# Optimization experiments

Measured on AMD Instinct MI355X. Metric: run time of the kernel, lower is better.

## Reference

```python
import jax, jax.numpy as jnp
import numpy as np

MIN_STD = 0.1

def _lin(x, W, b):
    return x @ W.T + b


def setup_inputs() -> dict:
    B, T, H, L, E, A = 256, 128, 2048, 256, 1024, 32
    key = jax.random.key(0)
    ks = jax.random.split(key, 40)
    def w(i, shape, s=0.02):
        return (jax.random.normal(ks[i], shape, jnp.float32) * s)
    z = lambda n: jnp.zeros((n,), jnp.float32)
    return {
        "prev_stochastic_state": w(0, (B, L), 1.0),
        "prev_hidden": w(1, (B, H), 1.0),
        "encoded_obs": w(2, (B, T, E), 1.0),
        "actions": w(3, (B, T, A), 1.0),
        "noise_prior": w(4, (B, T, L), 1.0),
        "noise_post": w(5, (B, T, L), 1.0),
        # fc_embed_state_action
        "W_embed": w(6, (H, L + A)), "b_embed": z(H),
        # GRUCell (torch layout: 3H rows = [r; z; n])
        "W_ih": w(7, (3 * H, H)), "b_ih": z(3 * H),
        "W_hh": w(8, (3 * H, H)), "b_hh": z(3 * H),
        # prior MLP (200-dim) + heads
        "Wp1": w(9, (200, H)), "bp1": z(200),
        "Wp2": w(10, (200, 200)), "bp2": z(200),
        "Wpm": w(11, (L, 200)), "bpm": z(L),
        "Wps": w(12, (L, 200)), "bps": z(L),
        # posterior MLP (200-dim) + heads
        "Wq1": w(13, (200, H + E)), "bq1": z(200),
        "Wq2": w(14, (200, 200)), "bq2": z(200),
        "Wqm": w(15, (L, 200)), "bqm": z(L),
        "Wqs": w(16, (L, 200)), "bqs": z(L),
        # reward head
        "Wr1": w(17, (200, L + H)), "br1": z(200),
        "Wr2": w(18, (200, 200)), "br2": z(200),
        "Wr3": w(19, (1, 200)), "br3": z(1),
    }


def reference(prev_stochastic_state, prev_hidden, encoded_obs, actions,
              noise_prior, noise_post,
              W_embed, b_embed, W_ih, b_ih, W_hh, b_hh,
              Wp1, bp1, Wp2, bp2, Wpm, bpm, Wps, bps,
              Wq1, bq1, Wq2, bq2, Wqm, bqm, Wqs, bqs,
              Wr1, br1, Wr2, br2, Wr3, br3):
    def gru(x, h):
        gi = x @ W_ih.T + b_ih          # [B, 3H]
        gh = h @ W_hh.T + b_hh
        i_r, i_z, i_n = jnp.split(gi, 3, axis=-1)
        h_r, h_z, h_n = jnp.split(gh, 3, axis=-1)
        r = jax.nn.sigmoid(i_r + h_r)
        z = jax.nn.sigmoid(i_z + h_z)
        n = jnp.tanh(i_n + r * h_n)
        return (1.0 - z) * n + z * h

    def step(carry, xs):
        post, h = carry
        enc_t, act_t, np_t, nq_t = xs
        emb = jax.nn.relu(_lin(jnp.concatenate([post, act_t], -1), W_embed, b_embed))
        h = gru(emb, h)
        pf = jax.nn.relu(_lin(jax.nn.relu(_lin(h, Wp1, bp1)), Wp2, bp2))
        pmu = _lin(pf, Wpm, bpm)
        pstd = jax.nn.softplus(_lin(pf, Wps, bps)) + MIN_STD
        prior_s = pmu + pstd * np_t
        qf = jax.nn.relu(_lin(jax.nn.relu(_lin(jnp.concatenate([h, enc_t], -1), Wq1, bq1)), Wq2, bq2))
        qmu = _lin(qf, Wqm, bqm)
        qstd = jax.nn.softplus(_lin(qf, Wqs, bqs)) + MIN_STD
        post = qmu + qstd * nq_t
        rew = _lin(jax.nn.relu(_lin(jax.nn.relu(_lin(jnp.concatenate([post, h], -1), Wr1, br1)), Wr2, br2)), Wr3, br3)
        return (post, h), (prior_s, post, h, pmu, pstd, qmu, qstd, rew)

    xs = (encoded_obs.transpose(1, 0, 2), actions.transpose(1, 0, 2),
          noise_prior.transpose(1, 0, 2), noise_post.transpose(1, 0, 2))
    _, ys = jax.lax.scan(step, (prev_stochastic_state, prev_hidden), xs)
    # scan stacks on axis 0 (time); torch stacks on dim 1 -> swap to [B, T, ...]
    return tuple(jnp.swapaxes(y, 0, 1) for y in ys)
```

## Files before the change

### kernel.cpp

```cpp
#include <hip/hip_runtime.h>
#include <hip/hip_bf16.h>

#define TS 128
#define NB 256
#define HD 2048
#define H3 6144
#define LD 256
#define ED 1024
#define AD 32
#define FD 200
#define KE 288
#define KQ 3072
#define KR 2304
#define MT 32768

typedef __attribute__((ext_vector_type(8))) short short8;
typedef __attribute__((ext_vector_type(4))) float f32x4;

constexpr size_t alup(size_t x) { return (x + 255) & ~size_t(255); }
constexpr size_t O_WE   = 0;
constexpr size_t O_WIH  = alup(O_WE   + 2ull*2048*288);
constexpr size_t O_WHH  = alup(O_WIH  + 2ull*6144*2048);
constexpr size_t O_WQ1  = alup(O_WHH  + 2ull*6144*2048);
constexpr size_t O_WQ2  = alup(O_WQ1  + 2ull*200*3072);
constexpr size_t O_WQMS = alup(O_WQ2  + 2ull*200*200);
constexpr size_t O_WP1  = alup(O_WQMS + 2ull*512*200);
constexpr size_t O_WP2  = alup(O_WP1  + 2ull*200*2048);
constexpr size_t O_WPMS = alup(O_WP2  + 2ull*200*200);
constexpr size_t O_WR1  = alup(O_WPMS + 2ull*512*200);
constexpr size_t O_WR2  = alup(O_WR1  + 2ull*200*2304);
constexpr size_t O_WR3  = alup(O_WR2  + 2ull*200*200);
constexpr size_t O_BQMS = alup(O_WR3  + 2ull*200);
constexpr size_t O_BPMS = alup(O_BQMS + 4ull*512);
constexpr size_t O_POSTB= alup(O_BPMS + 4ull*512);
constexpr size_t O_HB   = alup(O_POSTB+ 2ull*NB*LD);
constexpr size_t O_HF   = alup(O_HB   + 2ull*2*NB*HD);
constexpr size_t O_EMB  = alup(O_HF   + 4ull*2*NB*HD);
constexpr size_t O_Q1P  = alup(O_EMB  + 2ull*NB*HD);
constexpr size_t O_Q2   = alup(O_Q1P  + 4ull*4*NB*256);
constexpr size_t O_P1B  = alup(O_Q2   + 2ull*NB*FD);
constexpr size_t O_P2B  = alup(O_P1B  + 2ull*(size_t)MT*FD);
constexpr size_t O_END  = alup(O_P2B  + 2ull*(size_t)MT*FD);

#define Y0 0ull
#define Y1 8388608ull
#define Y2 16777216ull
#define Y3 83886080ull
#define Y4 92274688ull
#define Y5 100663296ull
#define Y6 109051904ull
#define Y7 117440512ull

__device__ __forceinline__ unsigned short f2bf(float f) {
  union { float f; unsigned u; } v; v.f = f;
  unsigned r = v.u + 0x7fffu + ((v.u >> 16) & 1u);
  return (unsigned short)(r >> 16);
}
__device__ __forceinline__ float bf2f(unsigned short u) {
  union { unsigned u; float f; } v; v.u = ((unsigned)u) << 16;
  return v.f;
}
__device__ __forceinline__ float sigm(float x) { return 1.f / (1.f + __expf(-x)); }
__device__ __forceinline__ float tanh_f(float x) {
  float e = __expf(-2.f * fabsf(x));
  float t = (1.f - e) / (1.f + e);
  return x >= 0.f ? t : -t;
}
__device__ __forceinline__ float softp(float x) { return x > 15.f ? x : log1pf(__expf(x)); }
__device__ __forceinline__ f32x4 z4() { f32x4 z; z[0]=0.f; z[1]=0.f; z[2]=0.f; z[3]=0.f; return z; }

struct SMem {
  alignas(16) short As[64*72];
  alignas(16) short Ws[128*72];
};
struct SMemG {
  alignas(16) short A[3][64*64];
  alignas(16) short W[3][64*64];
};

struct Aseg {
  const char* p0; int lda0; int K0; int f0;
  const char* p1; int lda1; int f1;
  int K;
};

__device__ __forceinline__ void stageA(short* As, const Aseg& a, int m0, int k0) {
  const int t = threadIdx.x;
  const int row = t >> 2;
  const int cb = (t & 3) << 4;
  #pragma unroll
  for (int i = 0; i < 2; ++i) {
    const int c = cb + i * 8;
    const int gk = k0 + c;
    short8 v = {};
    if (gk < a.K) {
      const char* p; long idx; int isf;
      if (gk < a.K0) { p = a.p0; idx = (long)(m0 + row) * a.lda0 + gk; isf = a.f0; }
      else           { p = a.p1; idx = (long)(m0 + row) * a.lda1 + (gk - a.K0); isf = a.f1; }
      if (isf) {
        const float* pf = (const float*)p + idx;
        #pragma unroll
        for (int j = 0; j < 8; ++j) v[j] = (short)f2bf(pf[j]);
      } else {
        v = *(const short8*)((const short*)p + idx);
      }
    }
    *(short8*)&As[row*72 + c] = v;
  }
}

__device__ __forceinline__ void stageW(short* Ws, const short* W, int ldw, int n0, int BN,
                                       int Nmax, int k0, int K) {
  const int nch = BN << 3;
  for (int id = threadIdx.x; id < nch; id += 256) {
    const int row = id >> 3;
    const int c = (id & 7) << 3;
    const int gk = k0 + c;
    int gr = n0 + row; gr = gr < Nmax ? gr : Nmax - 1;
    short8 v = {};
    if (gk < K) v = *(const short8*)(W + (long)gr * ldw + gk);
    *(short8*)&Ws[row*72 + c] = v;
  }
}

__device__ __forceinline__ void stageA_red(short* As, const float* q1p, const float* bq1,
                                           int m0, int k0) {
  const int t = threadIdx.x;
  const int row = t >> 2;
  const int cb = (t & 3) << 4;
  #pragma unroll
  for (int i = 0; i < 2; ++i) {
    const int c = cb + i * 8;
    const int gk = k0 + c;
    short8 v = {};
    if (gk < FD) {
      float s[8];
      #pragma unroll
      for (int j = 0; j < 8; ++j) s[j] = bq1[gk + j];
      #pragma unroll
      for (int ss = 0; ss < 4; ++ss) {
        const float* p = q1p + (size_t)ss * NB * 256 + (size_t)(m0 + row) * 256 + gk;
        #pragma unroll
        for (int j = 0; j < 8; ++j) s[j] += p[j];
      }
      #pragma unroll
      for (int j = 0; j < 8; ++j) v[j] = (short)f2bf(fmaxf(s[j], 0.f));
    }
    *(short8*)&As[row*72 + c] = v;
  }
}

template<int NF>
__device__ __forceinline__ void mma_tile(const short* As, const short* Ws, f32x4 acc[2][NF]) {
  const int lane = threadIdx.x & 63;
  const int w = threadIdx.x >> 6;
  const int wm = (w >> 1) << 5;
  const int wn = (w & 1) * (NF << 4);
  const int lr = lane & 15, lk = (lane >> 4) << 3;
  #pragma unroll
  for (int ks = 0; ks < 2; ++ks) {
    const int ko = ks * 32 + lk;
    short8 a0 = *(const short8*)&As[(wm + lr)*72 + ko];
    short8 a1 = *(const short8*)&As[(wm + 16 + lr)*72 + ko];
    #pragma unroll
    for (int f = 0; f < NF; ++f) {
      short8 b = *(const short8*)&Ws[(wn + f*16 + lr)*72 + ko];
      acc[0][f] = __builtin_amdgcn_mfma_f32_16x16x32_bf16(a0, b, acc[0][f], 0, 0, 0);
      acc[1][f] = __builtin_amdgcn_mfma_f32_16x16x32_bf16(a1, b, acc[1][f], 0, 0, 0);
    }
  }
}

template<int NF>
__device__ void run_gemm(SMem& sm, const Aseg& a, const short* W, int ldw, int m0, int n0,
                         int Nmax, f32x4 acc[2][NF], int kb, int ke) {
  for (int k0 = kb; k0 < ke; k0 += 64) {
    __syncthreads();
    stageA(sm.As, a, m0, k0);
    stageW(sm.Ws, W, ldw, n0, NF*32, Nmax, k0, a.K);
    __syncthreads();
    mma_tile<NF>(sm.As, sm.Ws, acc);
  }
}

template<int NF>
__device__ void epi_generic(f32x4 acc[2][NF], int m0, int n0, int Nmax, const float* bias,
                            int relu, float* outF, long rsF, unsigned short* outB, int rsB) {
  const int lane = threadIdx.x & 63;
  const int w = threadIdx.x >> 6;
  const int wm = (w >> 1) << 5, wn = (w & 1) * (NF << 4);
  #pragma unroll
  for (int mt = 0; mt < 2; ++mt)
  #pragma unroll
  for (int f = 0; f < NF; ++f)
  #pragma unroll
  for (int r = 0; r < 4; ++r) {
    const int m = m0 + wm + mt*16 + ((lane >> 4) << 2) + r;
    const int n = n0 + wn + f*16 + (lane & 15);
    if (n < Nmax) {
      float v = acc[mt][f][r];
      if (bias) v += bias[n];
      if (relu) v = fmaxf(v, 0.f);
      if (outF) outF[(long)m * rsF + n] = v;
      if (outB) outB[(long)m * rsB + n] = f2bf(v);
    }
  }
}

template<int NF>
__device__ void epi_heads(f32x4 acc[2][NF], int m0, int n0, const float* biasI,
                          const float* noise, long rs, float* outMu, float* outStd,
                          float* outComb, unsigned short* postbf) {
  const int lane = threadIdx.x & 63;
  const int w = threadIdx.x >> 6;
  const int wm = (w >> 1) << 5, wn = (w & 1) * (NF << 4);
  #pragma unroll
  for (int mt = 0; mt < 2; ++mt)
  #pragma unroll
  for (int f = 0; f < NF; ++f)
  #pragma unroll
  for (int r = 0; r < 4; ++r) {
    const int m = m0 + wm + mt*16 + ((lane >> 4) << 2) + r;
    const int n = n0 + wn + f*16 + (lane & 15);
    float v = acc[mt][f][r] + biasI[n];
    if (n & 1) v = softp(v) + 0.1f;
    float partner = __shfl_xor(v, 1);
    const int l = n >> 1;
    if (n & 1) {
      outStd[(long)m * rs + l] = v;
    } else {
      outMu[(long)m * rs + l] = v;
      float comb = v + partner * noise[(long)m * rs + l];
      outComb[(long)m * rs + l] = comb;
      if (postbf) postbf[m * LD + l] = f2bf(comb);
    }
  }
}

__device__ __forceinline__ void gl_lds16(const void* g, void* l) {
  __builtin_amdgcn_global_load_lds(
      (const __attribute__((address_space(1))) unsigned int*)g,
      (__attribute__((address_space(3))) unsigned int*)l, 16, 0, 0);
}

__device__ __forceinline__ void stage64(short* dst, const short* g, long ldw,
                                        int rbase, int k0) {
  const int w = threadIdx.x >> 6, l = threadIdx.x & 63;
  #pragma unroll
  for (int i = 0; i < 2; ++i) {
    const int inst = w*2 + i;
    const int row = inst*8 + (l >> 3);
    const int sc = (l & 7) ^ (row & 7);
    gl_lds16(g + (long)(rbase + row) * ldw + k0 + sc*8, dst + inst*512);
  }
}
__device__ __forceinline__ void stage_gi(short* dst, const short* W, int j0, int k0) {
  const int w = threadIdx.x >> 6, l = threadIdx.x & 63;
  #pragma unroll
  for (int i = 0; i < 2; ++i) {
    const int inst = w*2 + i;
    const int row = inst*8 + (l >> 3);
    const int g = (row >> 4) % 3;
    const int sc = (l & 7) ^ (row & 7);
    gl_lds16(W + (long)(g*2048 + j0 + (row & 15)) * 2048 + k0 + sc*8, dst + inst*512);
  }
}

__device__ __forceinline__ void mma_gi(const short* As, const short* Ws, f32x4 acc[3]) {
  const int lane = threadIdx.x & 63, w = threadIdx.x >> 6;
  const int lr = lane & 15, lk = (lane >> 4) << 3;
  #pragma unroll
  for (int ks = 0; ks < 2; ++ks) {
    const int ko = ks*32 + lk; const int ca = ko >> 3;
    const int ra = w*16 + lr;
    short8 av = *(const short8*)&As[ra*64 + ((ca ^ (ra & 7)) << 3)];
    #pragma unroll
    for (int f = 0; f < 3; ++f) {
      const int rb = f*16 + lr;
      short8 bv = *(const short8*)&Ws[rb*64 + ((ca ^ (rb & 7)) << 3)];
      acc[f] = __builtin_amdgcn_mfma_f32_16x16x32_bf16(av, bv, acc[f], 0, 0, 0);
    }
  }
}

struct CArgs {
  char* ws;
  const float* enc; const float* act; const float* nq;
  const float* b_e; const float* b_ih; const float* b_hh;
  const float* b_q1; const float* b_q2;
  float* y1; float* y2; float* y5; float* y6;
};

__device__ __forceinline__ void gruf_stage(SMemG& sm, int buf, int idx,
    const short* hB, const short* eB, const short* Whh, const short* Wih,
    int m0, int j0) {
  const short* Ab; const short* Wb; int k0;
  if (idx < 32) { Ab = hB; Wb = Whh; k0 = idx*64; }
  else          { Ab = eB; Wb = Wih; k0 = (idx-32)*64; }
  stage64(sm.A[buf], Ab, HD, m0, k0);
  stage_gi(sm.W[buf], Wb, j0, k0);
}

__global__ __launch_bounds__(256, 2) void k_gruf(CArgs A, int t) {
  __shared__ SMemG sm;
  const int id = blockIdx.x;
  const int xcd = id & 7, local = id >> 3;
  const int mi = local & 3, jl = local >> 2;
  const int m0 = mi << 6, j0 = xcd*256 + jl*16;
  const int p = t & 1;
  const short* hB  = (const short*)(A.ws + O_HB) + (size_t)p*NB*HD;
  const short* eB  = (const short*)(A.ws + O_EMB);
  const short* Whh = (const short*)(A.ws + O_WHH);
  const short* Wih = (const short*)(A.ws + O_WIH);
  f32x4 ah[3], ai[3];
  #pragma unroll
  for (int f = 0; f < 3; ++f) { ah[f] = z4(); ai[f] = z4(); }

  gruf_stage(sm, 0, 0, hB, eB, Whh, Wih, m0, j0);
  gruf_stage(sm, 1, 1, hB, eB, Whh, Wih, m0, j0);
  #pragma unroll 1
  for (int idx = 0; idx < 64; ++idx) {
    const int buf = idx % 3;
    if (idx + 2 < 64) {
      gruf_stage(sm, (idx + 2) % 3, idx + 2, hB, eB, Whh, Wih, m0, j0);
      asm volatile("s_waitcnt vmcnt(8)" ::: "memory");
    } else if (idx + 1 < 64) {
      asm volatile("s_waitcnt vmcnt(4)" ::: "memory");
    } else {
      asm volatile("s_waitcnt vmcnt(0)" ::: "memory");
    }
    __builtin_amdgcn_s_barrier();
    __builtin_amdgcn_sched_barrier(0);
    if (idx < 32) mma_gi(sm.A[buf], sm.W[buf], ah);
    else          mma_gi(sm.A[buf], sm.W[buf], ai);
    asm volatile("s_waitcnt lgkmcnt(0)" ::: "memory");
    __builtin_amdgcn_sched_barrier(0);
    __builtin_amdgcn_s_barrier();
  }

  const int lane = threadIdx.x & 63, w = threadIdx.x >> 6;
  const int lr = lane & 15;
  const int j = j0 + lr;
  const float* hFo = (const float*)(A.ws + O_HF) + (size_t)p*NB*HD;
  float*       hFn = (float*)(A.ws + O_HF) + (size_t)(p^1)*NB*HD;
  unsigned short* hBn = (unsigned short*)(A.ws + O_HB) + (size_t)(p^1)*NB*HD;
  #pragma unroll
  for (int r = 0; r < 4; ++r) {
    const int m = m0 + w*16 + ((lane >> 4) << 2) + r;
    const float ir = ai[0][r] + A.b_ih[j]        + ah[0][r] + A.b_hh[j];
    const float iz = ai[1][r] + A.b_ih[HD + j]   + ah[1][r] + A.b_hh[HD + j];
    const float in_ = ai[2][r] + A.b_ih[2*HD + j];
    const float hn  = ah[2][r] + A.b_hh[2*HD + j];
    const float rr = sigm(ir), zz = sigm(iz);
    const float nn = tanh_f(in_ + rr * hn);
    const float hv = (1.f - zz) * nn + zz * hFo[(size_t)m*HD + j];
    hFn[(size_t)m*HD + j] = hv;
    hBn[(size_t)m*HD + j] = f2bf(hv);
    A.y2[(size_t)m * (TS*HD) + (size_t)t*HD + j] = hv;
  }
}

__global__ __launch_bounds__(256, 2) void k_emb(CArgs A, int t) {
  __shared__ SMem sm;
  const int id = blockIdx.x;
  const int mi = id & 3, ni = id >> 2;
  const int m0 = mi << 6, n0 = ni << 7;
  Aseg a{A.ws + O_POSTB, LD, LD, 0, (const char*)(A.act + (size_t)t*AD), TS*AD, 1, KE};
  f32x4 acc[2][4];
  for (int i=0;i<2;++i) for (int j=0;j<4;++j) acc[i][j] = z4();
  run_gemm<4>(sm, a, (const short*)(A.ws + O_WE), KE, m0, n0, HD, acc, 0, 320);
  epi_generic<4>(acc, m0, n0, HD, A.b_e, 1, nullptr, 0, (unsigned short*)(A.ws + O_EMB), HD);
}

__global__ __launch_bounds__(256, 2) void k_q1(CArgs A, int t) {
  __shared__ SMem sm;
  const int id = blockIdx.x;
  const int s = id >> 3, rest = id & 7;
  const int mi = rest & 3, ni = rest >> 2;
  const int m0 = mi << 6, n0 = ni << 7;
  const short* hB = (const short*)(A.ws + O_HB) + (size_t)((t+1)&1)*NB*HD;
  Aseg a{(const char*)hB, HD, HD, 0, (const char*)(A.enc + (size_t)t*ED), TS*ED, 1, KQ};
  f32x4 acc[2][4];
  for (int i=0;i<2;++i) for (int j=0;j<4;++j) acc[i][j] = z4();
  run_gemm<4>(sm, a, (const short*)(A.ws + O_WQ1), KQ, m0, n0, FD, acc, s*768, s*768+768);
  epi_generic<4>(acc, m0, n0, FD, nullptr, 0,
                 (float*)(A.ws + O_Q1P) + (size_t)s*NB*256, 256, nullptr, 0);
}

__global__ __launch_bounds__(256, 2) void k_q2(CArgs A) {
  __shared__ SMem sm;
  const int id = blockIdx.x;
  const int mi = id & 3, ni = id >> 2;
  const int m0 = mi << 6, n0 = ni << 7;
  f32x4 acc[2][4];
  for (int i=0;i<2;++i) for (int j=0;j<4;++j) acc[i][j] = z4();
  const short* W = (const short*)(A.ws + O_WQ2);
  for (int k0 = 0; k0 < 256; k0 += 64) {
    __syncthreads();
    stageA_red(sm.As, (const float*)(A.ws + O_Q1P), A.b_q1, m0, k0);
    stageW(sm.Ws, W, FD, n0, 128, FD, k0, FD);
    __syncthreads();
    mma_tile<4>(sm.As, sm.Ws, acc);
  }
  epi_generic<4>(acc, m0, n0, FD, A.b_q2, 1, nullptr, 0, (unsigned short*)(A.ws + O_Q2), FD);
}

__global__ __launch_bounds__(256, 2) void k_heads(CArgs A, int t) {
  __shared__ SMem sm;
  const int id = blockIdx.x;
  const int mi = id & 3, ni = id >> 2;
  const int m0 = mi << 6, n0 = ni << 7;
  Aseg a{A.ws + O_Q2, FD, FD, 0, nullptr, 0, 0, FD};
  f32x4 acc[2][4];
  for (int i=0;i<2;++i) for (int j=0;j<4;++j) acc[i][j] = z4();
  run_gemm<4>(sm, a, (const short*)(A.ws + O_WQMS), FD, m0, n0, 512, acc, 0, 256);
  epi_heads<4>(acc, m0, n0, (const float*)(A.ws + O_BQMS),
               A.nq + (size_t)t*LD, (long)TS*LD,
               A.y5 + (size_t)t*LD, A.y6 + (size_t)t*LD, A.y1 + (size_t)t*LD,
               (unsigned short*)(A.ws + O_POSTB));
}

__global__ void k_init(char* ws, const float* prevs, const float* prevh,
  const float* We, const float* Wih, const float* Whh,
  const float* Wp1, const float* Wp2, const float* Wpm, const float* Wps,
  const float* Wq1, const float* Wq2, const float* Wqm, const float* Wqs,
  const float* Wr1, const float* Wr2, const float* Wr3,
  const float* bpm, const float* bps, const float* bqm, const float* bqs) {
  const size_t stride = (size_t)gridDim.x * blockDim.x;
  for (size_t i = (size_t)blockIdx.x*blockDim.x + threadIdx.x; i < 12582912ull; i += stride) {
    ((unsigned short*)(ws + O_WIH))[i] = f2bf(Wih[i]);
    ((unsigned short*)(ws + O_WHH))[i] = f2bf(Whh[i]);
    if (i < 589824)  ((unsigned short*)(ws + O_WE))[i]  = f2bf(We[i]);
    if (i < 614400)  ((unsigned short*)(ws + O_WQ1))[i] = f2bf(Wq1[i]);
    if (i < 409600)  ((unsigned short*)(ws + O_WP1))[i] = f2bf(Wp1[i]);
    if (i < 460800)  ((unsigned short*)(ws + O_WR1))[i] = f2bf(Wr1[i]);
    if (i < 40000) {
      ((unsigned short*)(ws + O_WQ2))[i] = f2bf(Wq2[i]);
      ((unsigned short*)(ws + O_WP2))[i] = f2bf(Wp2[i]);
      ((unsigned short*)(ws + O_WR2))[i] = f2bf(Wr2[i]);
    }
    if (i < 200) ((unsigned short*)(ws + O_WR3))[i] = f2bf(Wr3[i]);
    if (i < 102400) {
      const int r = (int)(i / 200), c = (int)(i % 200);
      ((unsigned short*)(ws + O_WQMS))[i] = f2bf(((r & 1) ? Wqs : Wqm)[(r >> 1)*200 + c]);
      ((unsigned short*)(ws + O_WPMS))[i] = f2bf(((r & 1) ? Wps : Wpm)[(r >> 1)*200 + c]);
    }
    if (i < 512) {
      ((float*)(ws + O_BQMS))[i] = ((i & 1) ? bqs : bqm)[i >> 1];
      ((float*)(ws + O_BPMS))[i] = ((i & 1) ? bps : bpm)[i >> 1];
    }
    if (i < 65536) ((unsigned short*)(ws + O_POSTB))[i] = f2bf(prevs[i]);
    if (i < 524288) {
      ((unsigned short*)(ws + O_HB))[i] = f2bf(prevh[i]);
      ((float*)(ws + O_HF))[i] = prevh[i];
    }
  }
}

__global__ __launch_bounds__(256, 2) void k_big(int mode, char* ws,
  const float* y1, const float* y2, float* y0, float* y3, float* y4,
  const float* npn, const float* bp1, const float* bp2, const float* br1, const float* br2) {
  __shared__ SMem sm;
  if (mode == 2) {
    for (int tile = blockIdx.x; tile < 2048; tile += gridDim.x) {
      const int mi = tile >> 2, ni = tile & 3;
      const int m0 = mi << 6, n0 = ni << 7;
      Aseg a{ws + O_P2B, FD, FD, 0, nullptr, 0, 0, FD};
      f32x4 acc[2][4];
      for (int i=0;i<2;++i) for (int j=0;j<4;++j) acc[i][j] = z4();
      run_gemm<4>(sm, a, (const short*)(ws + O_WPMS), FD, m0, n0, 512, acc, 0, 256);
      epi_heads<4>(acc, m0, n0, (const float*)(ws + O_BPMS), npn, 256, y3, y4, y0, nullptr);
    }
    return;
  }
  for (int tile = blockIdx.x; tile < 1024; tile += gridDim.x) {
    const int mi = tile >> 1, ni = tile & 1;
    const int m0 = mi << 6, n0 = ni << 7;
    Aseg a; const short* W; const float* bias;
    if (mode == 0)      { a = {(const char*)y2, HD, HD, 1, nullptr, 0, 0, HD}; W = (const short*)(ws + O_WP1); bias = bp1; }
    else if (mode == 1) { a = {ws + O_P1B, FD, FD, 0, nullptr, 0, 0, FD};      W = (const short*)(ws + O_WP2); bias = bp2; }
    else if (mode == 3) { a = {(const char*)y1, LD, LD, 1, (const char*)y2, HD, 1, KR}; W = (const short*)(ws + O_WR1); bias = br1; }
    else                { a = {ws + O_P1B, FD, FD, 0, nullptr, 0, 0, FD};      W = (const short*)(ws + O_WR2); bias = br2; }
    f32x4 acc[2][4];
    for (int i=0;i<2;++i) for (int j=0;j<4;++j) acc[i][j] = z4();
    const int ke = (a.K + 63) & ~63;
    run_gemm<4>(sm, a, W, a.K, m0, n0, FD, acc, 0, ke);
    unsigned short* outp = (unsigned short*)(ws + ((mode == 0 || mode == 3) ? O_P1B : O_P2B));
    epi_generic<4>(acc, m0, n0, FD, bias, 1, nullptr, 0, outp, FD);
  }
}

__global__ void k_r3(char* ws, const float* br3, float* y7) {
  __shared__ float w3[200];
  for (int i = threadIdx.x; i < 200; i += 256) w3[i] = bf2f(((unsigned short*)(ws + O_WR3))[i]);
  __syncthreads();
  const int m = blockIdx.x * 256 + threadIdx.x;
  const unsigned short* r2 = (const unsigned short*)(ws + O_P2B) + (size_t)m * FD;
  float s = br3[0];
  for (int k = 0; k < FD; k += 8) {
    short8 v = *(const short8*)(r2 + k);
    #pragma unroll
    for (int j = 0; j < 8; ++j) s += bf2f((unsigned short)v[j]) * w3[k + j];
  }
  y7[m] = s;
}

extern "C" void kernel_launch(void* const* d_in, const int* in_sizes, int n_in,
                              void* d_out, int out_size, void* d_ws, size_t ws_size,
                              hipStream_t stream) {
  (void)in_sizes; (void)n_in; (void)out_size; (void)ws_size;
  char* ws = (char*)d_ws;
  #define FIN(i) ((const float*)d_in[i])
  float* out = (float*)d_out;
  float* y0 = out + Y0; float* y1 = out + Y1; float* y2 = out + Y2; float* y3 = out + Y3;
  float* y4 = out + Y4; float* y5 = out + Y5; float* y6 = out + Y6; float* y7 = out + Y7;

  k_init<<<2048, 256, 0, stream>>>(ws, FIN(0), FIN(1), FIN(6), FIN(8), FIN(10),
    FIN(12), FIN(14), FIN(16), FIN(18), FIN(20), FIN(22), FIN(24), FIN(26),
    FIN(28), FIN(30), FIN(32), FIN(17), FIN(19), FIN(25), FIN(27));

  CArgs ca;
  ca.ws = ws; ca.enc = FIN(2); ca.act = FIN(3); ca.nq = FIN(5);
  ca.b_e = FIN(7); ca.b_ih = FIN(9); ca.b_hh = FIN(11); ca.b_q1 = FIN(21); ca.b_q2 = FIN(23);
  ca.y1 = y1; ca.y2 = y2; ca.y5 = y5; ca.y6 = y6;

  for (int t = 0; t < TS; ++t) {
    k_emb  <<<64,  256, 0, stream>>>(ca, t);
    k_gruf <<<512, 256, 0, stream>>>(ca, t);
    k_q1   <<<32,  256, 0, stream>>>(ca, t);
    k_q2   <<<8,   256, 0, stream>>>(ca);
    k_heads<<<16,  256, 0, stream>>>(ca, t);
  }

  k_big<<<2048, 256, 0, stream>>>(0, ws, y1, y2, y0, y3, y4, FIN(4), FIN(13), FIN(15), FIN(29), FIN(31));
  k_big<<<2048, 256, 0, stream>>>(1, ws, y1, y2, y0, y3, y4, FIN(4), FIN(13), FIN(15), FIN(29), FIN(31));
  k_big<<<2048, 256, 0, stream>>>(2, ws, y1, y2, y0, y3, y4, FIN(4), FIN(13), FIN(15), FIN(29), FIN(31));
  k_big<<<2048, 256, 0, stream>>>(3, ws, y1, y2, y0, y3, y4, FIN(4), FIN(13), FIN(15), FIN(29), FIN(31));
  k_big<<<2048, 256, 0, stream>>>(4, ws, y1, y2, y0, y3, y4, FIN(4), FIN(13), FIN(15), FIN(29), FIN(31));
  k_r3<<<128, 256, 0, stream>>>(ws, FIN(33), y7);
}
```

Before: 17.27 ms.

## Split GRU hidden GEMM off critical path and fuse posterior chain per step

The recurrent h@W_hh GEMM is moved into a separate pass that runs alongside a new fused per-row-block chain kernel (q1, q2, heads, next-step embedding), and it stores gh to a workspace buffer. The input-gate kernel then reads gh and only computes x@W_ih, using a W_ih layout permuted at init so each block streams contiguous rows. This cuts per-step launches from five to two and overlaps independent work, aiming to shorten the sequential critical path. In exchange it adds a large fp32 gh buffer that must be written and re-read every step, and the chain kernel uses few small blocks with long serial K loops.

```diff
diff --git a/kernel.cpp b/kernel.cpp
--- a/kernel.cpp
+++ b/kernel.cpp
@@ -36,9 +36,8 @@
 constexpr size_t O_HB   = alup(O_POSTB+ 2ull*NB*LD);
 constexpr size_t O_HF   = alup(O_HB   + 2ull*2*NB*HD);
 constexpr size_t O_EMB  = alup(O_HF   + 4ull*2*NB*HD);
-constexpr size_t O_Q1P  = alup(O_EMB  + 2ull*NB*HD);
-constexpr size_t O_Q2   = alup(O_Q1P  + 4ull*4*NB*256);
-constexpr size_t O_P1B  = alup(O_Q2   + 2ull*NB*FD);
+constexpr size_t O_GH   = alup(O_EMB  + 2ull*NB*HD);
+constexpr size_t O_P1B  = alup(O_GH   + 4ull*NB*H3);
 constexpr size_t O_P2B  = alup(O_P1B  + 2ull*(size_t)MT*FD);
 constexpr size_t O_END  = alup(O_P2B  + 2ull*(size_t)MT*FD);
 
@@ -77,6 +76,18 @@
   alignas(16) short A[3][64*64];
   alignas(16) short W[3][64*64];
 };
+struct SMemGi {
+  alignas(16) short A[3][64*64];
+  alignas(16) short W[3][48*64];
+};
+struct ChainC {
+  alignas(16) short Ws[256*40];
+  alignas(16) short q1f[16*264];
+  alignas(16) short q2f[16*264];
+  alignas(16) short postb[16*264];
+};
+union ChainSM { SMemG g; ChainC c; };
+union ProSM   { SMemG g; SMem legacy; };
 
 struct Aseg {
   const char* p0; int lda0; int K0; int f0;
@@ -123,33 +134,6 @@
   }
 }
 
-__device__ __forceinline__ void stageA_red(short* As, const float* q1p, const float* bq1,
-                                           int m0, int k0) {
-  const int t = threadIdx.x;
-  const int row = t >> 2;
-  const int cb = (t & 3) << 4;
-  #pragma unroll
-  for (int i = 0; i < 2; ++i) {
-    const int c = cb + i * 8;
-    const int gk = k0 + c;
-    short8 v = {};
-    if (gk < FD) {
-      float s[8];
-      #pragma unroll
-      for (int j = 0; j < 8; ++j) s[j] = bq1[gk + j];
-      #pragma unroll
-      for (int ss = 0; ss < 4; ++ss) {
-        const float* p = q1p + (size_t)ss * NB * 256 + (size_t)(m0 + row) * 256 + gk;
-        #pragma unroll
-        for (int j = 0; j < 8; ++j) s[j] += p[j];
-      }
-      #pragma unroll
-      for (int j = 0; j < 8; ++j) v[j] = (short)f2bf(fmaxf(s[j], 0.f));
-    }
-    *(short8*)&As[row*72 + c] = v;
-  }
-}
-
 template<int NF>
 __device__ __forceinline__ void mma_tile(const short* As, const short* Ws, f32x4 acc[2][NF]) {
   const int lane = threadIdx.x & 63;
@@ -254,15 +238,35 @@
     gl_lds16(g + (long)(rbase + row) * ldw + k0 + sc*8, dst + inst*512);
   }
 }
-__device__ __forceinline__ void stage_gi(short* dst, const short* W, int j0, int k0) {
+__device__ __forceinline__ void stage_giW(short* dst, const short* WX, int k0) {
   const int w = threadIdx.x >> 6, l = threadIdx.x & 63;
   #pragma unroll
-  for (int i = 0; i < 2; ++i) {
-    const int inst = w*2 + i;
-    const int row = inst*8 + (l >> 3);
-    const int g = (row >> 4) % 3;
+  for (int ii = 0; ii < 2; ++ii) {
+    const int i = (w < 3 ? w*2 : 4) + ii;
+    const int row = i*8 + (l >> 3);
     const int sc = (l & 7) ^ (row & 7);
-    gl_lds16(W + (long)(g*2048 + j0 + (row & 15)) * 2048 + k0 + sc*8, dst + inst*512);
+    gl_lds16(WX + (long)row * 2048 + k0 + sc*8, dst + i*512);
+  }
+}
+
+template<int NF>
+__device__ __forceinline__ void mma_swz(const short* As, const short* Ws, f32x4 acc[2][NF]) {
+  const int lane = threadIdx.x & 63, w = threadIdx.x >> 6;
+  const int wm = (w >> 1) << 5, wn = (w & 1) * (NF << 4);
+  const int lr = lane & 15, lk = (lane >> 4) << 3;
+  #pragma unroll
+  for (int ks = 0; ks < 2; ++ks) {
+    const int ko = ks*32 + lk; const int ca = ko >> 3;
+    const int ra0 = wm + lr, ra1 = wm + 16 + lr;
+    short8 a0 = *(const short8*)&As[ra0*64 + ((ca ^ (ra0 & 7)) << 3)];
+    short8 a1 = *(const short8*)&As[ra1*64 + ((ca ^ (ra1 & 7)) << 3)];
+    #pragma unroll
+    for (int f = 0; f < NF; ++f) {
+      const int rb = wn + f*16 + lr;
+      short8 b = *(const short8*)&Ws[rb*64 + ((ca ^ (rb & 7)) << 3)];
+      acc[0][f] = __builtin_amdgcn_mfma_f32_16x16x32_bf16(a0, b, acc[0][f], 0, 0, 0);
+      acc[1][f] = __builtin_amdgcn_mfma_f32_16x16x32_bf16(a1, b, acc[1][f], 0, 0, 0);
+    }
   }
 }
 
@@ -291,48 +295,64 @@
   float* y1; float* y2; float* y5; float* y6;
 };
 
-__device__ __forceinline__ void gruf_stage(SMemG& sm, int buf, int idx,
-    const short* hB, const short* eB, const short* Whh, const short* Wih,
-    int m0, int j0) {
-  const short* Ab; const short* Wb; int k0;
-  if (idx < 32) { Ab = hB; Wb = Whh; k0 = idx*64; }
-  else          { Ab = eB; Wb = Wih; k0 = (idx-32)*64; }
-  stage64(sm.A[buf], Ab, HD, m0, k0);
-  stage_gi(sm.W[buf], Wb, j0, k0);
-}
-
-__global__ __launch_bounds__(256, 2) void k_gruf(CArgs A, int t) {
-  __shared__ SMemG sm;
+__device__ void gh_pipe(SMemG& sm, const short* hB, const short* Whh, int m0, int n0,
+                        const float* bhh, float* ghout) {
+  f32x4 acc[2][2];
+  for (int i=0;i<2;++i) for (int j=0;j<2;++j) acc[i][j] = z4();
+  stage64(sm.A[0], hB, HD, m0, 0);   stage64(sm.W[0], Whh, HD, n0, 0);
+  stage64(sm.A[1], hB, HD, m0, 64);  stage64(sm.W[1], Whh, HD, n0, 64);
+  #pragma unroll 1
+  for (int idx = 0; idx < 32; ++idx) {
+    const int buf = idx % 3;
+    if (idx + 2 < 32) {
+      const int nb = (idx + 2) % 3;
+      stage64(sm.A[nb], hB, HD, m0, (idx+2)*64);
+      stage64(sm.W[nb], Whh, HD, n0, (idx+2)*64);
+      asm volatile("s_waitcnt vmcnt(8)" ::: "memory");
+    } else if (idx + 1 < 32) {
+      asm volatile("s_waitcnt vmcnt(4)" ::: "memory");
+    } else {
+      asm volatile("s_waitcnt vmcnt(0)" ::: "memory");
+    }
+    __builtin_amdgcn_s_barrier();
+    __builtin_amdgcn_sched_barrier(0);
+    mma_swz<2>(sm.A[buf], sm.W[buf], acc);
+    asm volatile("s_waitcnt lgkmcnt(0)" ::: "memory");
+    __builtin_amdgcn_sched_barrier(0);
+    __builtin_amdgcn_s_barrier();
+  }
+  epi_generic<2>(acc, m0, n0, H3, bhh, 0, ghout, H3, nullptr, 0);
+}
+
+__global__ __launch_bounds__(256, 2) void k_gi(CArgs A, int t) {
+  __shared__ SMemGi sm;
   const int id = blockIdx.x;
   const int xcd = id & 7, local = id >> 3;
   const int mi = local & 3, jl = local >> 2;
   const int m0 = mi << 6, j0 = xcd*256 + jl*16;
   const int p = t & 1;
-  const short* hB  = (const short*)(A.ws + O_HB) + (size_t)p*NB*HD;
   const short* eB  = (const short*)(A.ws + O_EMB);
-  const short* Whh = (const short*)(A.ws + O_WHH);
-  const short* Wih = (const short*)(A.ws + O_WIH);
-  f32x4 ah[3], ai[3];
-  #pragma unroll
-  for (int f = 0; f < 3; ++f) { ah[f] = z4(); ai[f] = z4(); }
-
-  gruf_stage(sm, 0, 0, hB, eB, Whh, Wih, m0, j0);
-  gruf_stage(sm, 1, 1, hB, eB, Whh, Wih, m0, j0);
+  const short* WX  = (const short*)(A.ws + O_WIH) + (size_t)(xcd*16 + jl)*48*2048;
+  f32x4 ai[3]; ai[0] = z4(); ai[1] = z4(); ai[2] = z4();
+
+  stage64(sm.A[0], eB, HD, m0, 0);   stage_giW(sm.W[0], WX, 0);
+  stage64(sm.A[1], eB, HD, m0, 64);  stage_giW(sm.W[1], WX, 64);
   #pragma unroll 1
-  for (int idx = 0; idx < 64; ++idx) {
+  for (int idx = 0; idx < 32; ++idx) {
     const int buf = idx % 3;
-    if (idx + 2 < 64) {
-      gruf_stage(sm, (idx + 2) % 3, idx + 2, hB, eB, Whh, Wih, m0, j0);
+    if (idx + 2 < 32) {
+      const int nb = (idx + 2) % 3;
+      stage64(sm.A[nb], eB, HD, m0, (idx+2)*64);
+      stage_giW(sm.W[nb], WX, (idx+2)*64);
       asm volatile("s_waitcnt vmcnt(8)" ::: "memory");
-    } else if (idx + 1 < 64) {
+    } else if (idx + 1 < 32) {
       asm volatile("s_waitcnt vmcnt(4)" ::: "memory");
     } else {
       asm volatile("s_waitcnt vmcnt(0)" ::: "memory");
     }
     __builtin_amdgcn_s_barrier();
     __builtin_amdgcn_sched_barrier(0);
-    if (idx < 32) mma_gi(sm.A[buf], sm.W[buf], ah);
-    else          mma_gi(sm.A[buf], sm.W[buf], ai);
+    mma_gi(sm.A[buf], sm.W[buf], ai);
     asm volatile("s_waitcnt lgkmcnt(0)" ::: "memory");
     __builtin_amdgcn_sched_barrier(0);
     __builtin_amdgcn_s_barrier();
@@ -344,15 +364,16 @@
   const float* hFo = (const float*)(A.ws + O_HF) + (size_t)p*NB*HD;
   float*       hFn = (float*)(A.ws + O_HF) + (size_t)(p^1)*NB*HD;
   unsigned short* hBn = (unsigned short*)(A.ws + O_HB) + (size_t)(p^1)*NB*HD;
+  const float* gh = (const float*)(A.ws + O_GH);
   #pragma unroll
   for (int r = 0; r < 4; ++r) {
     const int m = m0 + w*16 + ((lane >> 4) << 2) + r;
-    const float ir = ai[0][r] + A.b_ih[j]        + ah[0][r] + A.b_hh[j];
-    const float iz = ai[1][r] + A.b_ih[HD + j]   + ah[1][r] + A.b_hh[HD + j];
+    const float* g = gh + (size_t)m * H3;
+    const float ir  = ai[0][r] + A.b_ih[j]        + g[j];
+    const float iz  = ai[1][r] + A.b_ih[HD + j]   + g[HD + j];
     const float in_ = ai[2][r] + A.b_ih[2*HD + j];
-    const float hn  = ah[2][r] + A.b_hh[2*HD + j];
     const float rr = sigm(ir), zz = sigm(iz);
-    const float nn = tanh_f(in_ + rr * hn);
+    const float nn = tanh_f(in_ + rr * g[2*HD + j]);
     const float hv = (1.f - zz) * nn + zz * hFo[(size_t)m*HD + j];
     hFn[(size_t)m*HD + j] = hv;
     hBn[(size_t)m*HD + j] = f2bf(hv);
@@ -360,64 +381,222 @@
   }
 }
 
-__global__ __launch_bounds__(256, 2) void k_emb(CArgs A, int t) {
-  __shared__ SMem sm;
+struct W4 { short8 v[4]; };
+
+__device__ __forceinline__ void ldW(W4& r, const short* W, int ldw, int n0, int Nmax,
+                                    int k0, int K) {
+  const int tid = threadIdx.x;
+  #pragma unroll
+  for (int q = 0; q < 4; ++q) {
+    const int ch = q*256 + tid;
+    const int row = ch >> 2;
+    int gr = n0 + row; gr = gr < Nmax ? gr : Nmax - 1;
+    const int gk = k0 + (ch & 3) * 8;
+    short8 v = {};
+    if (gk < K) v = *(const short8*)(W + (long)gr*ldw + gk);
+    r.v[q] = v;
+  }
+}
+__device__ __forceinline__ void stW(short* Ws, const W4& r) {
+  const int tid = threadIdx.x;
+  #pragma unroll
+  for (int q = 0; q < 4; ++q) {
+    const int ch = q*256 + tid;
+    *(short8*)&Ws[(ch >> 2)*40 + (ch & 3)*8] = r.v[q];
+  }
+}
+
+template<int PH>
+__device__ __forceinline__ short8 ldA_chain(const CArgs& A, const short* lds,
+                                            const short* hB2, int m0, int t, int k0) {
+  const int lane = threadIdx.x & 63;
+  const int lr = lane & 15;
+  const int kk = k0 + ((lane >> 4) << 3);
+  if (PH == 1) {
+    if (kk < 2048) return *(const short8*)(hB2 + (long)(m0 + lr)*HD + kk);
+    const float* ep = A.enc + ((size_t)(m0 + lr)*TS + t)*ED + (kk - 2048);
+    f32x4 a = *(const f32x4*)ep;
+    f32x4 b = *(const f32x4*)(ep + 4);
+    short8 rv;
+    #pragma unroll
+    for (int j = 0; j < 4; ++j) { rv[j] = (short)f2bf(a[j]); rv[4+j] = (short)f2bf(b[j]); }
+    return rv;
+  }
+  if (PH == 4) {
+    if (kk < 256) return *(const short8*)&lds[lr*264 + kk];
+    const float* ap = A.act + ((size_t)(m0 + lr)*TS + (t + 1))*AD + (kk - 256);
+    f32x4 a = *(const f32x4*)ap;
+    f32x4 b = *(const f32x4*)(ap + 4);
+    short8 rv;
+    #pragma unroll
+    for (int j = 0; j < 4; ++j) { rv[j] = (short)f2bf(a[j]); rv[4+j] = (short)f2bf(b[j]); }
+    return rv;
+  }
+  return *(const short8*)&lds[lr*264 + kk];
+}
+
+__device__ __forceinline__ void mma_chain(const short* Ws, short8 af, f32x4 acc[4]) {
+  const int lane = threadIdx.x & 63, w = threadIdx.x >> 6;
+  const int lr = lane & 15;
+  #pragma unroll
+  for (int f = 0; f < 4; ++f) {
+    const int rb = w*64 + f*16 + lr;
+    short8 b = *(const short8*)&Ws[rb*40 + ((lane >> 4) << 3)];
+    acc[f] = __builtin_amdgcn_mfma_f32_16x16x32_bf16(af, b, acc[f], 0, 0, 0);
+  }
+}
+
+template<int PH>
+__device__ void chain_gemm(const CArgs& A, short* Ws, const short* aLDS, const short* hB2,
+                           int m0, int t, const short* W, int ldw, int Nmax,
+                           int S, int K, int n0, f32x4 acc[4]) {
+  W4 wrA, wrB;
+  ldW(wrA, W, ldw, n0, Nmax, 0, K);
+  if (S > 1) ldW(wrB, W, ldw, n0, Nmax, 32, K);
+  short8 af = ldA_chain<PH>(A, aLDS, hB2, m0, t, 0);
+  for (int s = 0; s < S; s += 2) {
+    {
+      __syncthreads();
+      stW(Ws, wrA);
+      __syncthreads();
+      if (s + 2 < S) ldW(wrA, W, ldw, n0, Nmax, (s+2)*32, K);
+      short8 afn = af;
+      if (s + 1 < S) afn = ldA_chain<PH>(A, aLDS, hB2, m0, t, (s+1)*32);
+      mma_chain(Ws, af, acc);
+      __builtin_amdgcn_sched_barrier(0);
+      af = afn;
+    }
+    if (s + 1 < S) {
+      __syncthreads();
+      stW(Ws, wrB);
+      __syncthreads();
+      if (s + 3 < S) ldW(wrB, W, ldw, n0, Nmax, (s+3)*32, K);
+      short8 afn = af;
+      if (s + 2 < S) afn = ldA_chain<PH>(A, aLDS, hB2, m0, t, (s+2)*32);
+      mma_chain(Ws, af, acc);
+      __builtin_amdgcn_sched_barrier(0);
+      af = afn;
+    }
+  }
+}
+
+__device__ __forceinline__ void epi_lds200(f32x4 acc[4], const float* bias, short* dst) {
+  const int lane = threadIdx.x & 63, w = threadIdx.x >> 6;
+  #pragma unroll
+  for (int f = 0; f < 4; ++f)
+  #pragma unroll
+  for (int r = 0; r < 4; ++r) {
+    const int n = w*64 + f*16 + (lane & 15);
+    const int mrow = ((lane >> 4) << 2) + r;
+    float v = acc[f][r] + (n < FD ? bias[n] : 0.f);
+    v = fmaxf(v, 0.f);
+    dst[mrow*264 + n] = (n < FD) ? (short)f2bf(v) : (short)0;
+  }
+}
+
+__global__ __launch_bounds__(256, 2) void k_chain(CArgs A, int t) {
+  __shared__ ChainSM sm;
   const int id = blockIdx.x;
-  const int mi = id & 3, ni = id >> 2;
-  const int m0 = mi << 6, n0 = ni << 7;
-  Aseg a{A.ws + O_POSTB, LD, LD, 0, (const char*)(A.act + (size_t)t*AD), TS*AD, 1, KE};
-  f32x4 acc[2][4];
-  for (int i=0;i<2;++i) for (int j=0;j<4;++j) acc[i][j] = z4();
-  run_gemm<4>(sm, a, (const short*)(A.ws + O_WE), KE, m0, n0, HD, acc, 0, 320);
-  epi_generic<4>(acc, m0, n0, HD, A.b_e, 1, nullptr, 0, (unsigned short*)(A.ws + O_EMB), HD);
-}
-
-__global__ __launch_bounds__(256, 2) void k_q1(CArgs A, int t) {
-  __shared__ SMem sm;
+  const int p2 = (t + 1) & 1;
+  const short* hB2 = (const short*)(A.ws + O_HB) + (size_t)p2*NB*HD;
+
+  if (id < 384) {
+    if (t == TS - 1) return;
+    const int xcd = id & 7, local = id >> 3;
+    const int mi = local & 3, nio = local >> 2;
+    const int m0 = mi << 6, n0 = xcd*768 + nio*64;
+    gh_pipe(sm.g, hB2, (const short*)(A.ws + O_WHH), m0, n0, A.b_hh,
+            (float*)(A.ws + O_GH));
+    return;
+  }
+
+  const int m0 = (id - 384) << 4;
+  short* Ws    = sm.c.Ws;
+  short* q1f   = sm.c.q1f;
+  short* q2f   = sm.c.q2f;
+  short* postb = sm.c.postb;
+  const int lane = threadIdx.x & 63, w = threadIdx.x >> 6;
+  f32x4 acc[4];
+
+  for (int f = 0; f < 4; ++f) acc[f] = z4();
+  chain_gemm<1>(A, Ws, nullptr, hB2, m0, t, (const short*)(A.ws + O_WQ1), KQ, FD, 96, KQ, 0, acc);
+  epi_lds200(acc, A.b_q1, q1f);
+  __syncthreads();
+
+  for (int f = 0; f < 4; ++f) acc[f] = z4();
+  chain_gemm<2>(A, Ws, q1f, hB2, m0, t, (const short*)(A.ws + O_WQ2), FD, FD, 7, FD, 0, acc);
+  epi_lds200(acc, A.b_q2, q2f);
+  __syncthreads();
+
+  const float* bqms = (const float*)(A.ws + O_BQMS);
+  #pragma unroll 1
+  for (int nc = 0; nc < 2; ++nc) {
+    for (int f = 0; f < 4; ++f) acc[f] = z4();
+    chain_gemm<3>(A, Ws, q2f, hB2, m0, t, (const short*)(A.ws + O_WQMS), FD, 512, 7, FD, nc*256, acc);
+    #pragma unroll
+    for (int f = 0; f < 4; ++f)
+    #pragma unroll
+    for (int r = 0; r < 4; ++r) {
+      const int n = nc*256 + w*64 + f*16 + (lane & 15);
+      const int mrow = ((lane >> 4) << 2) + r;
+      const int m = m0 + mrow;
+      float v = acc[f][r] + bqms[n];
+      if (n & 1) v = softp(v) + 0.1f;
+      float partner = __shfl_xor(v, 1);
+      const int l = n >> 1;
+      const size_t base = (size_t)m*TS*LD + (size_t)t*LD + l;
+      if (n & 1) {
+        A.y6[base] = v;
+      } else {
+        A.y5[base] = v;
+        float comb = v + partner * A.nq[base];
+        A.y1[base] = comb;
+        postb[mrow*264 + l] = (short)f2bf(comb);
+      }
+    }
+    __syncthreads();
+  }
+
+  if (t + 1 < TS) {
+    unsigned short* embp = (unsigned short*)(A.ws + O_EMB);
+    #pragma unroll 1
+    for (int nc = 0; nc < 8; ++nc) {
+      for (int f = 0; f < 4; ++f) acc[f] = z4();
+      chain_gemm<4>(A, Ws, postb, hB2, m0, t, (const short*)(A.ws + O_WE), KE, HD, 9, KE, nc*256, acc);
+      #pragma unroll
+      for (int f = 0; f < 4; ++f)
+      #pragma unroll
+      for (int r = 0; r < 4; ++r) {
+        const int n = nc*256 + w*64 + f*16 + (lane & 15);
+        const int mrow = ((lane >> 4) << 2) + r;
+        float v = acc[f][r] + A.b_e[n];
+        v = fmaxf(v, 0.f);
+        embp[(size_t)(m0 + mrow)*HD + n] = f2bf(v);
+      }
+      __syncthreads();
+    }
+  }
+}
+
+__global__ __launch_bounds__(256, 2) void k_pro(CArgs A) {
+  __shared__ ProSM sm;
   const int id = blockIdx.x;
-  const int s = id >> 3, rest = id & 7;
-  const int mi = rest & 3, ni = rest >> 2;
-  const int m0 = mi << 6, n0 = ni << 7;
-  const short* hB = (const short*)(A.ws + O_HB) + (size_t)((t+1)&1)*NB*HD;
-  Aseg a{(const char*)hB, HD, HD, 0, (const char*)(A.enc + (size_t)t*ED), TS*ED, 1, KQ};
-  f32x4 acc[2][4];
-  for (int i=0;i<2;++i) for (int j=0;j<4;++j) acc[i][j] = z4();
-  run_gemm<4>(sm, a, (const short*)(A.ws + O_WQ1), KQ, m0, n0, FD, acc, s*768, s*768+768);
-  epi_generic<4>(acc, m0, n0, FD, nullptr, 0,
-                 (float*)(A.ws + O_Q1P) + (size_t)s*NB*256, 256, nullptr, 0);
-}
-
-__global__ __launch_bounds__(256, 2) void k_q2(CArgs A) {
-  __shared__ SMem sm;
-  const int id = blockIdx.x;
-  const int mi = id & 3, ni = id >> 2;
-  const int m0 = mi << 6, n0 = ni << 7;
-  f32x4 acc[2][4];
-  for (int i=0;i<2;++i) for (int j=0;j<4;++j) acc[i][j] = z4();
-  const short* W = (const short*)(A.ws + O_WQ2);
-  for (int k0 = 0; k0 < 256; k0 += 64) {
-    __syncthreads();
-    stageA_red(sm.As, (const float*)(A.ws + O_Q1P), A.b_q1, m0, k0);
-    stageW(sm.Ws, W, FD, n0, 128, FD, k0, FD);
-    __syncthreads();
-    mma_tile<4>(sm.As, sm.Ws, acc);
-  }
-  epi_generic<4>(acc, m0, n0, FD, A.b_q2, 1, nullptr, 0, (unsigned short*)(A.ws + O_Q2), FD);
-}
-
-__global__ __launch_bounds__(256, 2) void k_heads(CArgs A, int t) {
-  __shared__ SMem sm;
-  const int id = blockIdx.x;
-  const int mi = id & 3, ni = id >> 2;
-  const int m0 = mi << 6, n0 = ni << 7;
-  Aseg a{A.ws + O_Q2, FD, FD, 0, nullptr, 0, 0, FD};
-  f32x4 acc[2][4];
-  for (int i=0;i<2;++i) for (int j=0;j<4;++j) acc[i][j] = z4();
-  run_gemm<4>(sm, a, (const short*)(A.ws + O_WQMS), FD, m0, n0, 512, acc, 0, 256);
-  epi_heads<4>(acc, m0, n0, (const float*)(A.ws + O_BQMS),
-               A.nq + (size_t)t*LD, (long)TS*LD,
-               A.y5 + (size_t)t*LD, A.y6 + (size_t)t*LD, A.y1 + (size_t)t*LD,
-               (unsigned short*)(A.ws + O_POSTB));
+  if (id < 384) {
+    const int xcd = id & 7, local = id >> 3;
+    const int mi = local & 3, nio = local >> 2;
+    const int m0 = mi << 6, n0 = xcd*768 + nio*64;
+    gh_pipe(sm.g, (const short*)(A.ws + O_HB), (const short*)(A.ws + O_WHH),
+            m0, n0, A.b_hh, (float*)(A.ws + O_GH));
+  } else {
+    const int e = id - 384;
+    const int mi = e & 3, ni = e >> 2;
+    const int m0 = mi << 6, n0 = ni << 7;
+    Aseg a{A.ws + O_POSTB, LD, LD, 0, (const char*)A.act, TS*AD, 1, KE};
+    f32x4 acc[2][4];
+    for (int i=0;i<2;++i) for (int j=0;j<4;++j) acc[i][j] = z4();
+    run_gemm<4>(sm.legacy, a, (const short*)(A.ws + O_WE), KE, m0, n0, HD, acc, 0, 320);
+    epi_generic<4>(acc, m0, n0, HD, A.b_e, 1, nullptr, 0, (unsigned short*)(A.ws + O_EMB), HD);
+  }
 }
 
 __global__ void k_init(char* ws, const float* prevs, const float* prevh,
@@ -428,7 +607,12 @@
   const float* bpm, const float* bps, const float* bqm, const float* bqs) {
   const size_t stride = (size_t)gridDim.x * blockDim.x;
   for (size_t i = (size_t)blockIdx.x*blockDim.x + threadIdx.x; i < 12582912ull; i += stride) {
-    ((unsigned short*)(ws + O_WIH))[i] = f2bf(Wih[i]);
+    {
+      const int row = (int)(i >> 11), col = (int)(i & 2047);
+      const int g = row >> 11, j = row & 2047;
+      const size_t nr = (size_t)((j >> 4)*48 + g*16 + (j & 15));
+      ((unsigned short*)(ws + O_WIH))[(nr << 11) + col] = f2bf(Wih[i]);
+    }
     ((unsigned short*)(ws + O_WHH))[i] = f2bf(Whh[i]);
     if (i < 589824)  ((unsigned short*)(ws + O_WE))[i]  = f2bf(We[i]);
     if (i < 614400)  ((unsigned short*)(ws + O_WQ1))[i] = f2bf(Wq1[i]);
@@ -524,12 +708,10 @@
   ca.b_e = FIN(7); ca.b_ih = FIN(9); ca.b_hh = FIN(11); ca.b_q1 = FIN(21); ca.b_q2 = FIN(23);
   ca.y1 = y1; ca.y2 = y2; ca.y5 = y5; ca.y6 = y6;
 
+  k_pro<<<448, 256, 0, stream>>>(ca);
   for (int t = 0; t < TS; ++t) {
-    k_emb  <<<64,  256, 0, stream>>>(ca, t);
-    k_gruf <<<512, 256, 0, stream>>>(ca, t);
-    k_q1   <<<32,  256, 0, stream>>>(ca, t);
-    k_q2   <<<8,   256, 0, stream>>>(ca);
-    k_heads<<<16,  256, 0, stream>>>(ca, t);
+    k_gi   <<<512, 256, 0, stream>>>(ca, t);
+    k_chain<<<400, 256, 0, stream>>>(ca, t);
   }
 
   k_big<<<2048, 256, 0, stream>>>(0, ws, y1, y2, y0, y3, y4, FIN(4), FIN(13), FIN(15), FIN(29), FIN(31));
```

Result: slower. 20.62 ms (+19.4%).
